# Optimization experiments

Measured on AMD Instinct MI355X. Metric: run time of the kernel, lower is better.

The kernel has to match this reference:

```python
import jax, jax.numpy as jnp
import numpy as np

B, H, W, C, NS = 4, 96, 96, 128, 2  # batch, height, width, dim, num_splits


def _layer_norm(x, g, b, eps=1e-5):
    m = x.mean(-1, keepdims=True)
    v = x.var(-1, keepdims=True)
    return (x - m) / jnp.sqrt(v + eps) * g + b


def _split_feature(x, ns):
    # [b,h,w,c] -> [b*ns*ns, h/ns, w/ns, c] (GMFlow split_feature, channel_last)
    b, h, w, c = x.shape
    return x.reshape(b, ns, h // ns, ns, w // ns, c).transpose(0, 1, 3, 2, 4, 5).reshape(b * ns * ns, h // ns, w // ns, c)


def _merge_splits(x, ns):
    bn, h, w, c = x.shape
    b = bn // (ns * ns)
    return x.reshape(b, ns, ns, h, w, c).transpose(0, 1, 3, 2, 4, 5).reshape(b, ns * h, ns * w, c)


def _shift_mask(h, w, ns):
    # standard Swin shifted-window additive mask: 0 within region, -100 across
    wh, ww = h // ns, w // ns
    sh, sw = wh // 2, ww // 2
    img = np.zeros((h, w), dtype=np.float32)
    cnt = 0
    for hs in (slice(0, -wh), slice(-wh, -sh), slice(-sh, None)):
        for wsl in (slice(0, -ww), slice(-ww, -sw), slice(-sw, None)):
            img[hs, wsl] = cnt
            cnt += 1
    win = img.reshape(ns, wh, ns, ww).transpose(0, 2, 1, 3).reshape(ns * ns, wh * ww)
    diff = win[:, None, :] - win[:, :, None]
    return jnp.asarray(np.where(diff != 0, -100.0, 0.0).astype(np.float32))


def setup_inputs():
    key = jax.random.key(0)
    ks = jax.random.split(key, 10)
    source = jax.random.normal(ks[0], (B, H * W, C), jnp.float32)
    sc = 1.0 / float(np.sqrt(C))
    return {
        "source": source,
        "target": source,  # self-attention branch: target == source
        "mask": _shift_mask(H, W, NS),
        "h": H, "w": W,
        "ln_g": 1.0 + 0.1 * jax.random.normal(ks[1], (C,), jnp.float32),
        "ln_b": 0.1 * jax.random.normal(ks[2], (C,), jnp.float32),
        "w_gq": sc * jax.random.normal(ks[3], (C, 2 * C), jnp.float32),
        "b_gq": 0.01 * jax.random.normal(ks[4], (2 * C,), jnp.float32),
        "w_kv": sc * jax.random.normal(ks[5], (C, 2 * C), jnp.float32),
        "b_kv": 0.01 * jax.random.normal(ks[6], (2 * C,), jnp.float32),
        "w_o1": sc * jax.random.normal(ks[7], (C, C), jnp.float32),
        "b_o1": 0.01 * jax.random.normal(ks[8], (C,), jnp.float32),
        "w_o2": sc * jax.random.normal(ks[9], (C, C), jnp.float32),
    }


def reference(source, target, mask, ln_g, ln_b, w_gq, b_gq, w_kv, b_kv, w_o1, b_o1, w_o2, h, w):
    # GatedAttentionUnit, nHead=1, self-attn, attn_type='swin', with_shift=True
    ns = NS
    b, seq, c = source.shape
    wh, ww = h // ns, w // ns
    sh, sw = wh // 2, ww // 2
    s = _layer_norm(source, ln_g, ln_b)
    t = _layer_norm(target, ln_g, ln_b)
    gate, Q = jnp.split(jax.nn.silu(s @ w_gq + b_gq), 2, axis=-1)
    K, V = jnp.split(jax.nn.silu(t @ w_kv + b_kv), 2, axis=-1)

    def win(x):
        x = jnp.roll(x.reshape(b, h, w, c), (-sh, -sw), axis=(1, 2))
        return _split_feature(x, ns).reshape(b * ns * ns, wh * ww, c)

    Qw, Kw, Vw = win(Q), win(K), win(V)
    # custom scaling: dim * full seq_len (not sqrt(d))
    scores = jnp.einsum('bic,bjc->bij', Qw, Kw) / (c * seq)
    scores = scores + jnp.tile(mask, (b, 1, 1))  # mask.repeat(b,1,1)
    attn = jax.nn.softmax(scores, axis=-1)
    out = jnp.einsum('bij,bjc->bic', attn, Vw).reshape(b * ns * ns, wh, ww, c)
    out = _merge_splits(out, ns)
    out = jnp.roll(out, (sh, sw), axis=(1, 2)).reshape(b, seq, c)
    out = out * gate  # multiplicative SiLU gate
    out = jax.nn.silu(out @ w_o1 + b_o1) @ w_o2
    y = out + source
    # torch's in-place += aliases both return values to out+res
    return (y, y)
```

## Files before the change

kernel.cpp:

```cpp
#include <hip/hip_runtime.h>

typedef short s8v __attribute__((ext_vector_type(8)));
typedef float f4v __attribute__((ext_vector_type(4)));

#define MFMA16(a,b,c) __builtin_amdgcn_mfma_f32_16x16x32_bf16(a,b,c,0,0,0)

#define TOK 36864
#define SEQ 9216
#define CH 128
#define WL 2304
#define ATTN_SCALE (1.0f/1179648.0f)

__device__ __forceinline__ float b2f(unsigned short u){
  union{unsigned i; float f;} c; c.i = ((unsigned)u)<<16; return c.f;
}
__device__ __forceinline__ unsigned short f2b(float f){
  union{float f; unsigned i;} c; c.f = f;
  unsigned r = c.i + 0x7fffu + ((c.i>>16)&1u);
  return (unsigned short)(r>>16);
}
__device__ __forceinline__ int wtok(int g, int pos){
  int bi = g>>2, ih = (g>>1)&1, iw = g&1;
  int rr = pos/48, ss = pos - rr*48;
  int p = ih*48 + rr, q = iw*48 + ss;
  int i = p + 24; if (i >= 96) i -= 96;
  int j = q + 24; if (j >= 96) j -= 96;
  return bi*SEQ + i*96 + j;
}

__global__ __launch_bounds__(256) void k_prep(const float* __restrict__ wgq,
    const float* __restrict__ wkv, const float* __restrict__ wo1, const float* __restrict__ wo2,
    const float* __restrict__ bgq, const float* __restrict__ bkv, const float* __restrict__ bo1,
    const float* __restrict__ lng, const float* __restrict__ lnb,
    unsigned short* __restrict__ Wt, unsigned short* __restrict__ Wt1,
    unsigned short* __restrict__ Wt2, unsigned short* __restrict__ P)
{
  int idx = blockIdx.x*256 + threadIdx.x;
  if (idx < 65536){
    int n = idx>>7, k = idx&127;
    Wt[idx] = f2b((n<256) ? wgq[k*256+n] : wkv[k*256+(n-256)]);
  } else if (idx < 81920){
    int t2 = idx-65536; int n = t2>>7, k = t2&127;
    Wt1[t2] = f2b(wo1[k*128+n]);
  } else if (idx < 98304){
    int t2 = idx-81920; int n = t2>>7, k = t2&127;
    Wt2[t2] = f2b(wo2[k*128+n]);
  } else if (idx < 99200){
    int j = idx-98304;
    float v;
    if (j<256)      v = bgq[j];
    else if (j<512) v = bkv[j-256];
    else if (j<640) v = bo1[j-512];
    else if (j<768) v = lng[j-640];
    else            v = lnb[j-768];
    P[j] = f2b(v);
  }
}

__global__ __launch_bounds__(256) void k_proj(const float* __restrict__ src,
    const unsigned short* __restrict__ Wt, const unsigned short* __restrict__ P,
    float* __restrict__ gate, unsigned short* __restrict__ Qw,
    unsigned short* __restrict__ Kw, unsigned short* __restrict__ Vb)
{
  __shared__ __align__(16) short lS[64][136];
  const int tid = threadIdx.x;
  const int w = tid>>6, l = tid&63, l16 = l&15, quad = l>>4;
  const int m0 = blockIdx.x*64;

  {
    int row = tid>>2, lam = tid&3;
    const float* sp = src + (m0+row)*CH + lam*32;
    float v[32]; float s = 0.f, sq = 0.f;
#pragma unroll
    for (int j=0;j<32;j++){ v[j] = sp[j]; s += v[j]; sq += v[j]*v[j]; }
    s += __shfl_xor(s,1); sq += __shfl_xor(sq,1);
    s += __shfl_xor(s,2); sq += __shfl_xor(sq,2);
    float mean = s*(1.f/128.f);
    float rstd = rsqrtf(sq*(1.f/128.f) - mean*mean + 1e-5f);
#pragma unroll
    for (int j=0;j<32;j++){
      int c = lam*32 + j;
      lS[row][c] = (short)f2b((v[j]-mean)*rstd*b2f(P[640+c]) + b2f(P[768+c]));
    }
  }
  __syncthreads();

  s8v a[4];
#pragma unroll
  for (int kc=0;kc<4;kc++) a[kc] = *(const s8v*)&lS[w*16+l16][kc*32+quad*8];

  int tokv[4], gidx[4], posv[4];
#pragma unroll
  for (int r=0;r<4;r++){
    int token = m0 + w*16 + quad*4 + r;
    int bi = token / SEQ; int t = token - bi*SEQ;
    int i = t / 96; int j = t - i*96;
    int p = i - 24; if (p<0) p += 96;
    int q = j - 24; if (q<0) q += 96;
    int ihh = (p>=48); int rr = p - ihh*48;
    int iww = (q>=48); int ss = q - iww*48;
    tokv[r] = token;
    gidx[r] = bi*4 + ihh*2 + iww;
    posv[r] = rr*48 + ss;
  }

#pragma unroll
  for (int chunk=0; chunk<2; chunk++){
    f4v acc[16];
#pragma unroll
    for (int nt=0;nt<16;nt++){
      f4v z = {0.f,0.f,0.f,0.f}; acc[nt] = z;
      const unsigned short* bp = Wt + (chunk*256 + nt*16 + l16)*CH + quad*8;
#pragma unroll
      for (int kc=0;kc<4;kc++)
        acc[nt] = MFMA16(a[kc], *(const s8v*)(bp + kc*32), acc[nt]);
    }
#pragma unroll
    for (int nt=0;nt<16;nt++){
      int col = chunk*256 + nt*16 + l16;
      float bias = b2f(P[col]);
#pragma unroll
      for (int r=0;r<4;r++){
        float z = acc[nt][r] + bias;
        z = z / (1.0f + __expf(-z));
        if (col < 128){
          gate[tokv[r]*CH + col] = z;
        } else if (col < 256){
          Qw[(gidx[r]*WL + posv[r])*CH + (col-128)] = f2b(z);
        } else if (col < 384){
          Kw[(gidx[r]*WL + posv[r])*CH + (col-256)] = f2b(z);
        } else {
          Vb[tokv[r]*CH + (col-384)] = f2b(z);
        }
      }
    }
  }
}

__global__ __launch_bounds__(256) void k_vt(const unsigned short* __restrict__ Vb,
    unsigned short* __restrict__ Vt)
{
  __shared__ short lR[64*66];
  const int tid = threadIdx.x;
  const int g = blockIdx.y;
  const int q0 = blockIdx.x*64;
  const int lane = tid&63, grp = tid>>6;
#pragma unroll 4
  for (int p=0;p<16;p++){
    int key = p*4 + grp;
    int token = wtok(g, q0+key);
    unsigned v = *(const unsigned*)(Vb + token*CH + lane*2);
    *(unsigned*)&lR[key*66 + lane*2] = v;
  }
  __syncthreads();
#pragma unroll 8
  for (int i=0;i<32;i++){
    int ch = grp*32 + i;
    Vt[g*CH*WL + ch*WL + q0 + lane] = (unsigned short)lR[lane*66 + ch];
  }
}

__global__ __launch_bounds__(256, 3) void k_attn(const unsigned short* Qw,
    const unsigned short* __restrict__ Kw, const unsigned short* __restrict__ Vt,
    unsigned short* attn)
{
  __shared__ __align__(16) short lK[64][136];
  __shared__ __align__(16) short lV[128][72];
  __shared__ __align__(16) short lP[4][16][72];
  const int tid = threadIdx.x;
  const int w = tid>>6, l = tid&63, l16 = l&15, quad = l>>4;

  const int n  = blockIdx.x;
  const int L  = (n & 7)*72 + (n >> 3);
  const int g  = L/36;
  const int q0 = (L - g*36)*64;
  const int ih = (g>>1)&1, iw = g&1;

  const unsigned short* qp = Qw + (g*WL + q0 + w*16 + l16)*CH + quad*8;
  s8v aQ[4];
#pragma unroll
  for (int kc=0;kc<4;kc++) aQ[kc] = *(const s8v*)(qp + kc*32);

  int qrl[4], qcl[4];
#pragma unroll
  for (int r=0;r<4;r++){
    int qpj = q0 + w*16 + quad*4 + r;
    int qr = qpj/48, qs = qpj - qr*48;
    qrl[r] = (qr>=24); qcl[r] = (qs>=24);
  }

  const int kr0 = tid>>4, kc0 = (tid&15)*8;
  const int vc0 = tid>>3, vp0 = (tid&7)*8;
  const unsigned short* Kbase = Kw + g*WL*CH;
  const unsigned short* Vbase = Vt + g*CH*WL;
  s8v rK[4], rV[4];

#define LOAD_TILE(kk) do { \
    const unsigned short* Kg_ = Kbase + (kk)*CH; \
    const unsigned short* Vg_ = Vbase + (kk); \
    rK[0] = *(const s8v*)(Kg_ + (kr0+ 0)*CH + kc0); \
    rK[1] = *(const s8v*)(Kg_ + (kr0+16)*CH + kc0); \
    rK[2] = *(const s8v*)(Kg_ + (kr0+32)*CH + kc0); \
    rK[3] = *(const s8v*)(Kg_ + (kr0+48)*CH + kc0); \
    rV[0] = *(const s8v*)(Vg_ + (vc0+ 0)*WL + vp0); \
    rV[1] = *(const s8v*)(Vg_ + (vc0+32)*WL + vp0); \
    rV[2] = *(const s8v*)(Vg_ + (vc0+64)*WL + vp0); \
    rV[3] = *(const s8v*)(Vg_ + (vc0+96)*WL + vp0); \
  } while(0)

#define WRITE_TILE() do { \
    *(s8v*)&lK[kr0+ 0][kc0] = rK[0]; \
    *(s8v*)&lK[kr0+16][kc0] = rK[1]; \
    *(s8v*)&lK[kr0+32][kc0] = rK[2]; \
    *(s8v*)&lK[kr0+48][kc0] = rK[3]; \
    *(s8v*)&lV[vc0+ 0][vp0] = rV[0]; \
    *(s8v*)&lV[vc0+32][vp0] = rV[1]; \
    *(s8v*)&lV[vc0+64][vp0] = rV[2]; \
    *(s8v*)&lV[vc0+96][vp0] = rV[3]; \
  } while(0)

  f4v O[8];
#pragma unroll
  for (int i=0;i<8;i++){ f4v z = {0.f,0.f,0.f,0.f}; O[i] = z; }
  float lsum[4] = {0.f,0.f,0.f,0.f};

  LOAD_TILE(0);

  for (int k0=0; k0<WL; k0+=64){
    __syncthreads();
    WRITE_TILE();
    __syncthreads();
    if (k0+64 < WL) LOAD_TILE(k0+64);

    f4v S[4];
#pragma unroll
    for (int nt=0;nt<4;nt++){
      f4v z = {0.f,0.f,0.f,0.f}; S[nt] = z;
#pragma unroll
      for (int kc=0;kc<4;kc++)
        S[nt] = MFMA16(aQ[kc], *(const s8v*)&lK[nt*16+l16][kc*32+quad*8], S[nt]);
    }

#pragma unroll
    for (int nt=0;nt<4;nt++){
      int key = k0 + nt*16 + l16;
      int kr = key/48, ks = key - kr*48;
      int krl = (kr>=24), kcl = (ks>=24);
#pragma unroll
      for (int r=0;r<4;r++){
        bool masked = (ih && (krl != qrl[r])) || (iw && (kcl != qcl[r]));
        float p = masked ? 0.0f : __expf(S[nt][r]*ATTN_SCALE);
        unsigned short pb = f2b(p);
        lsum[r] += b2f(pb);
        lP[w][quad*4+r][nt*16+l16] = (short)pb;
      }
    }
    asm volatile("s_waitcnt lgkmcnt(0)" ::: "memory");

#pragma unroll
    for (int kc2=0;kc2<2;kc2++){
      s8v aP = *(const s8v*)&lP[w][l16][kc2*32+quad*8];
#pragma unroll
      for (int nt=0;nt<8;nt++)
        O[nt] = MFMA16(aP, *(const s8v*)&lV[nt*16+l16][kc2*32+quad*8], O[nt]);
    }
  }

#undef LOAD_TILE
#undef WRITE_TILE

#pragma unroll
  for (int r=0;r<4;r++){
#pragma unroll
    for (int m=1;m<16;m<<=1) lsum[r] += __shfl_xor(lsum[r], m);
  }
  unsigned short* outp = attn + (g*WL + q0 + w*16)*CH;
#pragma unroll
  for (int nt=0;nt<8;nt++){
#pragma unroll
    for (int r=0;r<4;r++)
      outp[(quad*4+r)*CH + nt*16 + l16] = f2b(O[nt][r] / lsum[r]);
  }
}

__global__ __launch_bounds__(256) void k_out(const unsigned short* __restrict__ attn,
    const unsigned short* __restrict__ Wo1, const unsigned short* __restrict__ P,
    const unsigned short* __restrict__ Wo2, const float* __restrict__ src,
    float* out)
{
  __shared__ __align__(16) short lA[64][136];
  __shared__ __align__(16) short lU[4][16][136];
  const int tid = threadIdx.x;
  const int w = tid>>6, l = tid&63, l16 = l&15, quad = l>>4;
  const int m0 = blockIdx.x*64;
  {
    int r_loc = tid>>2;
    int cb = (tid&3)*32;
    int token = m0 + r_loc;
    int bi = token / SEQ; int t = token - bi*SEQ;
    int i = t / 96; int j = t - i*96;
    int p = i - 24; if (p<0) p += 96;
    int q = j - 24; if (q<0) q += 96;
    int ihh = (p>=48); int rr = p - ihh*48;
    int iww = (q>=48); int ss = q - iww*48;
    int wb = (bi*4 + ihh*2 + iww)*WL + rr*48 + ss;
    const unsigned short* av = attn + wb*CH + cb;
    const float* gv = out + token*CH + cb;
#pragma unroll
    for (int u=0;u<4;u++){
      s8v a8 = *(const s8v*)(av + u*8);
      float4 g0 = *(const float4*)(gv + u*8);
      float4 g1 = *(const float4*)(gv + u*8 + 4);
      s8v o;
      o[0]=(short)f2b(b2f((unsigned short)a8[0])*g0.x);
      o[1]=(short)f2b(b2f((unsigned short)a8[1])*g0.y);
      o[2]=(short)f2b(b2f((unsigned short)a8[2])*g0.z);
      o[3]=(short)f2b(b2f((unsigned short)a8[3])*g0.w);
      o[4]=(short)f2b(b2f((unsigned short)a8[4])*g1.x);
      o[5]=(short)f2b(b2f((unsigned short)a8[5])*g1.y);
      o[6]=(short)f2b(b2f((unsigned short)a8[6])*g1.z);
      o[7]=(short)f2b(b2f((unsigned short)a8[7])*g1.w);
      *(s8v*)&lA[r_loc][cb + u*8] = o;
    }
  }
  __syncthreads();

  s8v aA[4];
#pragma unroll
  for (int kc=0;kc<4;kc++) aA[kc] = *(const s8v*)&lA[w*16+l16][kc*32+quad*8];
  f4v acc[8];
#pragma unroll
  for (int nt=0;nt<8;nt++){
    f4v z = {0.f,0.f,0.f,0.f}; acc[nt] = z;
    const unsigned short* bp = Wo1 + (nt*16+l16)*CH + quad*8;
#pragma unroll
    for (int kc=0;kc<4;kc++) acc[nt] = MFMA16(aA[kc], *(const s8v*)(bp + kc*32), acc[nt]);
  }
#pragma unroll
  for (int nt=0;nt<8;nt++){
    int col = nt*16 + l16;
    float bias = b2f(P[512+col]);
#pragma unroll
    for (int r=0;r<4;r++){
      float z = acc[nt][r] + bias;
      z = z / (1.0f + __expf(-z));
      lU[w][quad*4+r][col] = (short)f2b(z);
    }
  }
  __syncthreads();

  s8v aU[4];
#pragma unroll
  for (int kc=0;kc<4;kc++) aU[kc] = *(const s8v*)&lU[w][l16][kc*32+quad*8];
  f4v acc2[8];
#pragma unroll
  for (int nt=0;nt<8;nt++){
    f4v z = {0.f,0.f,0.f,0.f}; acc2[nt] = z;
    const unsigned short* bp = Wo2 + (nt*16+l16)*CH + quad*8;
#pragma unroll
    for (int kc=0;kc<4;kc++) acc2[nt] = MFMA16(aU[kc], *(const s8v*)(bp + kc*32), acc2[nt]);
  }
#pragma unroll
  for (int nt=0;nt<8;nt++){
#pragma unroll
    for (int r=0;r<4;r++){
      int token = m0 + w*16 + quad*4 + r;
      int col = nt*16 + l16;
      float y = acc2[nt][r] + src[token*CH + col];
      out[token*CH + col] = y;
      out[TOK*CH + token*CH + col] = y;
    }
  }
}

extern "C" void kernel_launch(void* const* d_in, const int* in_sizes, int n_in,
                              void* d_out, int out_size, void* d_ws, size_t ws_size,
                              hipStream_t stream)
{
  const float* src = (const float*)d_in[0];
  const float* lng = (const float*)d_in[5];
  const float* lnb = (const float*)d_in[6];
  const float* wgq = (const float*)d_in[7];
  const float* bgq = (const float*)d_in[8];
  const float* wkv = (const float*)d_in[9];
  const float* bkv = (const float*)d_in[10];
  const float* wo1 = (const float*)d_in[11];
  const float* bo1 = (const float*)d_in[12];
  const float* wo2 = (const float*)d_in[13];

  char* ws = (char*)d_ws;
  unsigned short* P   = (unsigned short*)(ws);
  unsigned short* Wt  = (unsigned short*)(ws + 2048);
  unsigned short* Wt1 = (unsigned short*)(ws + 133120);
  unsigned short* Wt2 = (unsigned short*)(ws + 165888);
  unsigned short* Qw  = (unsigned short*)(ws + 198656);
  unsigned short* Kw  = (unsigned short*)(ws + 9635840);
  unsigned short* Vt  = (unsigned short*)(ws + 19073024);
  unsigned short* Vb  = (unsigned short*)(ws + 28510208);
  float* out = (float*)d_out;

  k_prep<<<dim3(388),   dim3(256), 0, stream>>>(wgq, wkv, wo1, wo2, bgq, bkv, bo1, lng, lnb,
                                                Wt, Wt1, Wt2, P);
  k_proj<<<dim3(576),   dim3(256), 0, stream>>>(src, Wt, P, out, Qw, Kw, Vb);
  k_vt  <<<dim3(36,16), dim3(256), 0, stream>>>(Vb, Vt);
  k_attn<<<dim3(576),   dim3(256), 0, stream>>>(Qw, Kw, Vt, Qw);
  k_out <<<dim3(576),   dim3(256), 0, stream>>>(Qw, Wt1, P, Wt2, src, out);
}
```

Measured before the change: 355.6 us.

## Double queries per attention block to reuse K/V tiles across two row groups

```diff
diff --git a/kernel.cpp b/kernel.cpp
--- a/kernel.cpp
+++ b/kernel.cpp
@@ -160,33 +160,38 @@
   }
 }
 
-__global__ __launch_bounds__(256, 3) void k_attn(const unsigned short* Qw,
+__global__ __launch_bounds__(256, 2) void k_attn(const unsigned short* Qw,
     const unsigned short* __restrict__ Kw, const unsigned short* __restrict__ Vt,
     unsigned short* attn)
 {
   __shared__ __align__(16) short lK[64][136];
   __shared__ __align__(16) short lV[128][72];
-  __shared__ __align__(16) short lP[4][16][72];
+  __shared__ __align__(16) short lP[4][32][72];
   const int tid = threadIdx.x;
   const int w = tid>>6, l = tid&63, l16 = l&15, quad = l>>4;
 
   const int n  = blockIdx.x;
-  const int L  = (n & 7)*72 + (n >> 3);
-  const int g  = L/36;
-  const int q0 = (L - g*36)*64;
+  const int L  = (n & 7)*36 + (n >> 3);
+  const int g  = L/18;
+  const int q0 = (L - g*18)*128;
   const int ih = (g>>1)&1, iw = g&1;
 
-  const unsigned short* qp = Qw + (g*WL + q0 + w*16 + l16)*CH + quad*8;
-  s8v aQ[4];
-#pragma unroll
-  for (int kc=0;kc<4;kc++) aQ[kc] = *(const s8v*)(qp + kc*32);
-
-  int qrl[4], qcl[4];
+  s8v aQ[2][4];
+#pragma unroll
+  for (int h=0; h<2; h++){
+    const unsigned short* qp = Qw + (g*WL + q0 + w*32 + h*16 + l16)*CH + quad*8;
+#pragma unroll
+    for (int kc=0;kc<4;kc++) aQ[h][kc] = *(const s8v*)(qp + kc*32);
+  }
+
+  int qrl[2][4], qcl[2][4];
+#pragma unroll
+  for (int h=0; h<2; h++)
 #pragma unroll
   for (int r=0;r<4;r++){
-    int qpj = q0 + w*16 + quad*4 + r;
+    int qpj = q0 + w*32 + h*16 + quad*4 + r;
     int qr = qpj/48, qs = qpj - qr*48;
-    qrl[r] = (qr>=24); qcl[r] = (qs>=24);
+    qrl[h][r] = (qr>=24); qcl[h][r] = (qs>=24);
   }
 
   const int kr0 = tid>>4, kc0 = (tid&15)*8;
@@ -219,10 +224,12 @@
     *(s8v*)&lV[vc0+96][vp0] = rV[3]; \
   } while(0)
 
-  f4v O[8];
-#pragma unroll
-  for (int i=0;i<8;i++){ f4v z = {0.f,0.f,0.f,0.f}; O[i] = z; }
-  float lsum[4] = {0.f,0.f,0.f,0.f};
+  f4v O[2][8];
+#pragma unroll
+  for (int h=0;h<2;h++)
+#pragma unroll
+  for (int i=0;i<8;i++){ f4v z = {0.f,0.f,0.f,0.f}; O[h][i] = z; }
+  float lsum[2][4] = {{0.f,0.f,0.f,0.f},{0.f,0.f,0.f,0.f}};
 
   LOAD_TILE(0);
 
@@ -232,37 +239,47 @@
     __syncthreads();
     if (k0+64 < WL) LOAD_TILE(k0+64);
 
-    f4v S[4];
+    f4v S[2][4];
 #pragma unroll
     for (int nt=0;nt<4;nt++){
-      f4v z = {0.f,0.f,0.f,0.f}; S[nt] = z;
-#pragma unroll
-      for (int kc=0;kc<4;kc++)
-        S[nt] = MFMA16(aQ[kc], *(const s8v*)&lK[nt*16+l16][kc*32+quad*8], S[nt]);
-    }
-
-#pragma unroll
-    for (int nt=0;nt<4;nt++){
-      int key = k0 + nt*16 + l16;
-      int kr = key/48, ks = key - kr*48;
-      int krl = (kr>=24), kcl = (ks>=24);
-#pragma unroll
-      for (int r=0;r<4;r++){
-        bool masked = (ih && (krl != qrl[r])) || (iw && (kcl != qcl[r]));
-        float p = masked ? 0.0f : __expf(S[nt][r]*ATTN_SCALE);
-        unsigned short pb = f2b(p);
-        lsum[r] += b2f(pb);
-        lP[w][quad*4+r][nt*16+l16] = (short)pb;
+      f4v z = {0.f,0.f,0.f,0.f}; S[0][nt] = z; S[1][nt] = z;
+#pragma unroll
+      for (int kc=0;kc<4;kc++){
+        s8v bK = *(const s8v*)&lK[nt*16+l16][kc*32+quad*8];
+        S[0][nt] = MFMA16(aQ[0][kc], bK, S[0][nt]);
+        S[1][nt] = MFMA16(aQ[1][kc], bK, S[1][nt]);
       }
     }
+
+#pragma unroll
+    for (int h=0;h<2;h++){
+#pragma unroll
+      for (int nt=0;nt<4;nt++){
+        int key = k0 + nt*16 + l16;
+        int kr = key/48, ks = key - kr*48;
+        int krl = (kr>=24), kcl = (ks>=24);
+#pragma unroll
+        for (int r=0;r<4;r++){
+          bool masked = (ih && (krl != qrl[h][r])) || (iw && (kcl != qcl[h][r]));
+          float p = masked ? 0.0f : __expf(S[h][nt][r]*ATTN_SCALE);
+          unsigned short pb = f2b(p);
+          lsum[h][r] += b2f(pb);
+          lP[w][h*16+quad*4+r][nt*16+l16] = (short)pb;
+        }
+      }
+    }
     asm volatile("s_waitcnt lgkmcnt(0)" ::: "memory");
 
 #pragma unroll
     for (int kc2=0;kc2<2;kc2++){
-      s8v aP = *(const s8v*)&lP[w][l16][kc2*32+quad*8];
-#pragma unroll
-      for (int nt=0;nt<8;nt++)
-        O[nt] = MFMA16(aP, *(const s8v*)&lV[nt*16+l16][kc2*32+quad*8], O[nt]);
+      s8v aP0 = *(const s8v*)&lP[w][     l16][kc2*32+quad*8];
+      s8v aP1 = *(const s8v*)&lP[w][16 + l16][kc2*32+quad*8];
+#pragma unroll
+      for (int nt=0;nt<8;nt++){
+        s8v bV = *(const s8v*)&lV[nt*16+l16][kc2*32+quad*8];
+        O[0][nt] = MFMA16(aP0, bV, O[0][nt]);
+        O[1][nt] = MFMA16(aP1, bV, O[1][nt]);
+      }
     }
   }
 
@@ -270,16 +287,20 @@
 #undef WRITE_TILE
 
 #pragma unroll
+  for (int h=0;h<2;h++)
+#pragma unroll
   for (int r=0;r<4;r++){
 #pragma unroll
-    for (int m=1;m<16;m<<=1) lsum[r] += __shfl_xor(lsum[r], m);
-  }
-  unsigned short* outp = attn + (g*WL + q0 + w*16)*CH;
+    for (int m=1;m<16;m<<=1) lsum[h][r] += __shfl_xor(lsum[h][r], m);
+  }
+  unsigned short* outp = attn + (g*WL + q0 + w*32)*CH;
+#pragma unroll
+  for (int h=0;h<2;h++)
 #pragma unroll
   for (int nt=0;nt<8;nt++){
 #pragma unroll
     for (int r=0;r<4;r++)
-      outp[(quad*4+r)*CH + nt*16 + l16] = f2b(O[nt][r] / lsum[r]);
+      outp[(h*16+quad*4+r)*CH + nt*16 + l16] = f2b(O[h][nt][r] / lsum[h][r]);
   }
 }
 
@@ -403,6 +424,6 @@
                                                 Wt, Wt1, Wt2, P);
   k_proj<<<dim3(576),   dim3(256), 0, stream>>>(src, Wt, P, out, Qw, Kw, Vb);
   k_vt  <<<dim3(36,16), dim3(256), 0, stream>>>(Vb, Vt);
-  k_attn<<<dim3(576),   dim3(256), 0, stream>>>(Qw, Kw, Vt, Qw);
+  k_attn<<<dim3(288),   dim3(256), 0, stream>>>(Qw, Kw, Vt, Qw);
   k_out <<<dim3(576),   dim3(256), 0, stream>>>(Qw, Wt1, P, Wt2, src, out);
 }
```

Result: no change. 362.0 us (+1.8%).
